# Performance work log

Hardware: AMD Instinct MI355X
Metric: run time of the kernel (lower is better)

The kernel has to match this reference:

```python
import jax, jax.numpy as jnp
import numpy as np

VOCAB = 32000
UNITS = 1024


def setup_inputs() -> dict:
    key = jax.random.key(0)
    ks = jax.random.split(key, 8)
    B, S, U = 64, 256, UNITS
    x = jax.random.randint(ks[0], (B, S), 0, VOCAB)
    emb = jax.random.normal(ks[1], (VOCAB, U), dtype=jnp.float32) * 0.02
    def gru_params(k):
        k1, k2, k3 = jax.random.split(k, 3)
        kernel = jax.random.normal(k1, (U, 3 * U), dtype=jnp.float32) * (1.0 / np.sqrt(U))
        rec_kernel = jax.random.normal(k2, (U, 3 * U), dtype=jnp.float32) * (1.0 / np.sqrt(U))
        bias = jnp.zeros((2, 3 * U), dtype=jnp.float32)  # reset_after=True: input bias + recurrent bias
        return kernel, rec_kernel, bias
    kf, rf, bf = gru_params(ks[2])
    kb, rb, bb = gru_params(ks[3])
    return {"x": x, "emb": emb,
            "kernel_fwd": kf, "rec_fwd": rf, "bias_fwd": bf,
            "kernel_bwd": kb, "rec_bwd": rb, "bias_bwd": bb}


def _gru(x_emb, mask, kernel, rec_kernel, bias, reverse):
    # Keras GRU, reset_after=True: z,r,hh gates; mask_zero copy-through state.
    if reverse:
        x_emb = x_emb[:, ::-1]
        mask = mask[:, ::-1]
    B, S, U = x_emb.shape
    b_i, b_r = bias[0], bias[1]
    # precompute input projections for all timesteps: [S, B, 3U]
    xp = (jnp.einsum('bsu,uh->bsh', x_emb, kernel) + b_i).transpose(1, 0, 2)
    mask_t = mask.transpose(1, 0)  # [S, B]

    def step(h, inp):
        xp_t, m_t = inp
        rec = h @ rec_kernel + b_r
        xz, xr, xh = jnp.split(xp_t, 3, axis=-1)
        rz, rr, rh = jnp.split(rec, 3, axis=-1)
        z = jax.nn.sigmoid(xz + rz)
        r = jax.nn.sigmoid(xr + rr)
        hh = jnp.tanh(xh + r * rh)
        h_new = z * h + (1.0 - z) * hh
        h = jnp.where(m_t[:, None], h_new, h)  # masked steps carry state/output through
        return h, h

    h0 = jnp.zeros((B, U), dtype=x_emb.dtype)
    _, outs = jax.lax.scan(step, h0, (xp, mask_t))
    outs = outs.transpose(1, 0, 2)  # [B, S, U]
    if reverse:
        outs = outs[:, ::-1]
    return outs


def reference(x, emb, kernel_fwd, rec_fwd, bias_fwd, kernel_bwd, rec_bwd, bias_bwd):
    mask = x != 0  # Embedding(mask_zero=True)
    x_emb = emb[x]  # [B, S, U]
    out_f = _gru(x_emb, mask, kernel_fwd, rec_fwd, bias_fwd, reverse=False)
    out_b = _gru(x_emb, mask, kernel_bwd, rec_bwd, bias_bwd, reverse=True)
    return out_f + out_b  # merge_mode='sum'
```

## Files before the change

### kernel.cpp

```cpp
#include <hip/hip_runtime.h>

typedef __bf16 bf16;
typedef __bf16 bf16x8 __attribute__((ext_vector_type(8)));
typedef __bf16 bf16x4 __attribute__((ext_vector_type(4)));
typedef float f32x4 __attribute__((ext_vector_type(4)));

static constexpr size_t SZ_RT   = 2ull*3072*1024*2;
static constexpr size_t SZ_XP   = 2ull*16384*3072*2;
static constexpr size_t SZ_MASK = 16384ull*4;
static constexpr size_t SLOT    = 2ull*8192*16;
static constexpr size_t OFF_RT   = 0;
static constexpr size_t OFF_XP   = OFF_RT + SZ_RT;
static constexpr size_t OFF_MASK = OFF_XP + SZ_XP;
static constexpr size_t OFF_BAR  = OFF_MASK + SZ_MASK;
static constexpr size_t OFF_RING = OFF_BAR + 2048;
static constexpr size_t OFF_KT   = OFF_RING;
static constexpr size_t OFF_XE   = OFF_RING + 2ull*3072*1024*2;

__global__ void zero_ws_k(char* ws) {
  size_t i = (size_t)blockIdx.x*256 + threadIdx.x;
  if (i < SLOT/16)                  ((uint4*)(ws + OFF_RING))[i] = make_uint4(0u,0u,0u,0u);
  else if (i < SLOT/16 + 128)       ((uint4*)(ws + OFF_BAR))[i - SLOT/16] = make_uint4(0u,0u,0u,0u);
}

__global__ void transpose_cast_k(const float* kf, const float* kb,
                                 const float* rf, const float* rb, char* ws) {
  __shared__ float tile[32][33];
  const int mat = blockIdx.z;
  const float* src = (mat==0)?kf:(mat==1)?kb:(mat==2)?rf:rb;
  bf16* dst = (bf16*)(ws + ((mat<2)?OFF_KT:OFF_RT)) + (size_t)(mat&1)*3072*1024;
  const int k0 = blockIdx.x*32, n0 = blockIdx.y*32;
  const int r = threadIdx.x >> 5, c = threadIdx.x & 31;
  for (int rr = r; rr < 32; rr += 8)
    tile[rr][c] = src[(size_t)(k0+rr)*3072 + n0 + c];
  __syncthreads();
  const int rn = threadIdx.x >> 3, kq = threadIdx.x & 7;
  bf16x4 v;
  #pragma unroll
  for (int ii = 0; ii < 4; ++ii) v[ii] = (bf16)tile[kq*4+ii][rn];
  *(bf16x4*)(dst + (size_t)(n0+rn)*1024 + k0 + kq*4) = v;
}

__global__ void gather_xe_k(const int* x, const float* emb, char* ws) {
  size_t c = (size_t)blockIdx.x*256 + threadIdx.x;
  int rowid = (int)(c >> 7); int u8 = (int)(c & 127);
  int t = rowid >> 6, b = rowid & 63;
  int tok = x[b*256 + t];
  const float* e = emb + (size_t)tok*1024 + u8*8;
  float4 a  = *(const float4*)e;
  float4 b2 = *(const float4*)(e+4);
  bf16x8 o;
  o[0]=(bf16)a.x;  o[1]=(bf16)a.y;  o[2]=(bf16)a.z;  o[3]=(bf16)a.w;
  o[4]=(bf16)b2.x; o[5]=(bf16)b2.y; o[6]=(bf16)b2.z; o[7]=(bf16)b2.w;
  *(bf16x8*)((bf16*)(ws+OFF_XE) + (size_t)rowid*1024 + u8*8) = o;
}

__global__ void make_mask_k(const int* x, char* ws) {
  int tid = blockIdx.x*256 + threadIdx.x;
  int t = tid >> 6, b = tid & 63;
  ((float*)(ws+OFF_MASK))[tid] = (x[b*256+t] != 0) ? 1.0f : 0.0f;
}

__device__ __forceinline__ void async16(void* lds, const void* g) {
  __builtin_amdgcn_global_load_lds((const __attribute__((address_space(1))) unsigned int*)g,
                                   (__attribute__((address_space(3))) unsigned int*)lds,
                                   16, 0, 0);
}

__global__ __launch_bounds__(256) void xp_gemm_k(const float* bias_f, const float* bias_b, char* ws) {
  __shared__ __align__(16) char smem[16384];
  const int tid = threadIdx.x, w = tid>>6, l = tid&63;
  const int m0 = blockIdx.x*128, n0 = blockIdx.y*128, d = blockIdx.z;
  const bf16* xe = (const bf16*)(ws + OFF_XE);
  const bf16* Bt = (const bf16*)(ws + OFF_KT) + (size_t)d*3072*1024;
  const float* bias = d ? bias_b : bias_f;
  const int wm = (w>>1)*64, wn = (w&1)*64;
  const f32x4 fzero = {0.f,0.f,0.f,0.f};
  f32x4 acc[4][4];
  #pragma unroll
  for (int i=0;i<4;++i)
    #pragma unroll
    for (int jj=0;jj<4;++jj) acc[i][jj] = fzero;
  for (int k0 = 0; k0 < 1024; k0 += 32) {
    #pragma unroll
    for (int it = 0; it < 2; ++it) {
      int cc = w*128 + it*64 + l;
      int row = cc>>2, kp = cc&3;
      async16(smem        + (size_t)(w*128 + it*64)*16, xe + (size_t)(m0+row)*1024 + k0 + kp*8);
      async16(smem + 8192 + (size_t)(w*128 + it*64)*16, Bt + (size_t)(n0+row)*1024 + k0 + kp*8);
    }
    __builtin_amdgcn_s_waitcnt(0);
    __syncthreads();
    const bf16* As = (const bf16*)smem;
    const bf16* Bs = (const bf16*)(smem + 8192);
    bf16x8 bfr[4];
    #pragma unroll
    for (int nt=0;nt<4;++nt)
      bfr[nt] = *(const bf16x8*)(Bs + (wn + nt*16 + (l&15))*32 + (l>>4)*8);
    #pragma unroll
    for (int mt=0;mt<4;++mt) {
      bf16x8 af = *(const bf16x8*)(As + (wm + mt*16 + (l&15))*32 + (l>>4)*8);
      #pragma unroll
      for (int nt=0;nt<4;++nt)
        acc[mt][nt] = __builtin_amdgcn_mfma_f32_16x16x32_bf16(af, bfr[nt], acc[mt][nt], 0,0,0);
    }
    __syncthreads();
  }
  bf16* xp = (bf16*)(ws + OFF_XP);
  #pragma unroll
  for (int nt=0;nt<4;++nt) {
    int n = n0 + wn + nt*16 + (l&15);
    float bv = bias[n];
    int g = n>>10, jj = (n>>4)&63, u = n&15;
    #pragma unroll
    for (int mt=0;mt<4;++mt) {
      #pragma unroll
      for (int r2=0;r2<4;++r2) {
        int m = m0 + wm + mt*16 + (l>>4)*4 + r2;
        int t = m>>6, b = m&63;
        float val = acc[mt][nt][r2] + bv;
        xp[((((size_t)(d*64+jj)*256 + t)*3 + g)*64 + b)*16 + u] = (bf16)val;
      }
    }
  }
}

__global__ __launch_bounds__(256, 1) void gru_scan_k(char* ws,
                                                     const float* bias_f, const float* bias_b) {
  __shared__ __align__(16) float parts[2*4*3*64*20];
  const int wg = blockIdx.x;
  const int d = wg >> 6, j = wg & 63;
  const int tid = threadIdx.x, w = tid >> 6, l = tid & 63;
  const bf16* rT    = (const bf16*)(ws + OFF_RT) + (size_t)d*3072*1024;
  const char* xp    = (const char*)(ws + OFF_XP);
  const float* mask = (const float*)(ws + OFF_MASK);
  char* ring = ws + OFF_RING;
  unsigned* flags = (unsigned*)(ws + OFF_BAR);
  const float* bias = d ? bias_b : bias_f;
  const f32x4 fzero = {0.f,0.f,0.f,0.f};

  const int b = tid >> 2, uq = tid & 3;

  f32x4 br[3];
  #pragma unroll
  for (int g = 0; g < 3; ++g)
    br[g] = *(const f32x4*)(bias + 3072 + g*1024 + j*16 + uq*4);

  const int kt0 = w*8;
  bf16x8 Breg[24];
  #pragma unroll
  for (int g = 0; g < 3; ++g)
    #pragma unroll
    for (int kk = 0; kk < 8; ++kk)
      Breg[g*8+kk] = *(const bf16x8*)(rT + (size_t)(g*1024 + j*16 + (l&15))*1024
                                         + (kt0+kk)*32 + (l>>4)*8);

  float hold[4] = {0.f, 0.f, 0.f, 0.f};

  const int wq = (j&1)*2 + (uq>>1);
  const int chunk = ((j>>1)*4 + (b>>4))*64 + ((b & 15) | (wq << 4));
  const int coff = chunk*16 + (uq&1)*8;

  const unsigned fidx = (unsigned)(d*256 + w*64 + l);

  bf16x4 xz_c, xr_c, xh_c; float m_c;
  {
    const int t0 = d ? 255 : 0;
    const char* xpt = xp + ((size_t)(d*64 + j)*256 + t0)*6144;
    xz_c = *(const bf16x4*)(xpt +        tid*8);
    xr_c = *(const bf16x4*)(xpt + 2048 + tid*8);
    xh_c = *(const bf16x4*)(xpt + 4096 + tid*8);
    m_c  = mask[t0*64 + b];
  }

  for (int step = 0; step < 256; ++step) {
    const int t = d ? (255 - step) : step;
    {
      unsigned v = __hip_atomic_load(&flags[fidx], __ATOMIC_RELAXED, __HIP_MEMORY_SCOPE_AGENT);
      while (!__all((int)(v >= (unsigned)step))) {
        __builtin_amdgcn_s_sleep(2);
        v = __hip_atomic_load(&flags[fidx], __ATOMIC_RELAXED, __HIP_MEMORY_SCOPE_AGENT);
      }
    }
    const char* hsrc = ring + (size_t)step*SLOT + (size_t)d*(SLOT/2);
    f32x4 acc[4][3];
    #pragma unroll
    for (int mt=0;mt<4;++mt) { acc[mt][0]=fzero; acc[mt][1]=fzero; acc[mt][2]=fzero; }
    bf16x8 aP[4], aN[4];
    #pragma unroll
    for (int mt=0;mt<4;++mt)
      aP[mt] = *(const bf16x8*)(hsrc + ((size_t)(kt0*4 + mt)*64 + l)*16);
    #pragma unroll
    for (int kk = 0; kk < 8; ++kk) {
      if (kk < 7) {
        #pragma unroll
        for (int mt=0;mt<4;++mt)
          aN[mt] = *(const bf16x8*)(hsrc + ((size_t)((kt0+kk+1)*4 + mt)*64 + l)*16);
      }
      #pragma unroll
      for (int mt = 0; mt < 4; ++mt) {
        acc[mt][0] = __builtin_amdgcn_mfma_f32_16x16x32_bf16(aP[mt], Breg[0*8+kk], acc[mt][0],0,0,0);
        acc[mt][1] = __builtin_amdgcn_mfma_f32_16x16x32_bf16(aP[mt], Breg[1*8+kk], acc[mt][1],0,0,0);
        acc[mt][2] = __builtin_amdgcn_mfma_f32_16x16x32_bf16(aP[mt], Breg[2*8+kk], acc[mt][2],0,0,0);
      }
      if (kk < 7) {
        #pragma unroll
        for (int mt=0;mt<4;++mt) aP[mt] = aN[mt];
      }
    }
    {
      float* pw = parts + ((size_t)((step&1)*4 + w)*3)*1280;
      #pragma unroll
      for (int mt = 0; mt < 4; ++mt)
        #pragma unroll
        for (int g = 0; g < 3; ++g)
          #pragma unroll
          for (int r2 = 0; r2 < 4; ++r2)
            pw[g*1280 + (mt*16 + (l>>4)*4 + r2)*20 + (l&15)] = acc[mt][g][r2];
    }
    __syncthreads();
    f32x4 rec0 = br[0], rec1 = br[1], rec2 = br[2];
    {
      const float* pb = parts + (size_t)(step&1)*4*3*1280 + b*20 + uq*4;
      #pragma unroll
      for (int w2 = 0; w2 < 4; ++w2) {
        rec0 += *(const f32x4*)(pb + (w2*3+0)*1280);
        rec1 += *(const f32x4*)(pb + (w2*3+1)*1280);
        rec2 += *(const f32x4*)(pb + (w2*3+2)*1280);
      }
    }
    f32x4 hv;
    #pragma unroll
    for (int i = 0; i < 4; ++i) {
      float z = 1.f/(1.f + __expf(-((float)xz_c[i] + rec0[i])));
      float r = 1.f/(1.f + __expf(-((float)xr_c[i] + rec1[i])));
      float pre = (float)xh_c[i] + r*rec2[i];
      pre = fminf(fmaxf(pre, -15.f), 15.f);
      float e2 = __expf(-2.f*pre);
      float hh = (1.f - e2)/(1.f + e2);
      float hn = z*hold[i] + (1.f - z)*hh;
      float ho = (m_c != 0.f) ? hn : hold[i];
      hold[i] = ho;
      hv[i] = ho;
    }
    if (step < 255) {
      union { bf16 h4[4]; unsigned long long q; } pk;
      #pragma unroll
      for (int i = 0; i < 4; ++i) pk.h4[i] = (bf16)hv[i];
      char* hdst = ring + (size_t)(step+1)*SLOT + (size_t)d*(SLOT/2);
      __hip_atomic_store((unsigned long long*)(hdst + coff), pk.q,
                         __ATOMIC_RELAXED, __HIP_MEMORY_SCOPE_AGENT);
      __builtin_amdgcn_s_waitcnt(0);
      asm volatile("" ::: "memory");
      if ((tid & 63) == 0)
        __hip_atomic_store(&flags[d*256 + j*4 + w], (unsigned)(step+1),
                           __ATOMIC_RELAXED, __HIP_MEMORY_SCOPE_AGENT);
    }
    {
      float* slab = (float*)(ws + OFF_XP + ((size_t)(d*64 + j)*256 + t)*6144);
      *(f32x4*)(slab + tid*4) = hv;
    }
    if (step < 255) {
      const int tn = d ? (254 - step) : (step + 1);
      const char* xpn = xp + ((size_t)(d*64 + j)*256 + tn)*6144;
      xz_c = *(const bf16x4*)(xpn +        tid*8);
      xr_c = *(const bf16x4*)(xpn + 2048 + tid*8);
      xh_c = *(const bf16x4*)(xpn + 4096 + tid*8);
      m_c  = mask[tn*64 + b];
    }
  }
}

__global__ void add_out_k(const char* ws, float* out) {
  size_t i = (size_t)blockIdx.x*256 + threadIdx.x;
  int uqq = (int)(i & 3), j = (int)((i>>2) & 63), t = (int)((i>>8) & 255), b = (int)(i >> 16);
  const float* pf = (const float*)(ws + OFF_XP + ((size_t)(     j)*256 + t)*6144);
  const float* pb = (const float*)(ws + OFF_XP + ((size_t)(64 + j)*256 + t)*6144);
  f32x4 a = *(const f32x4*)(pf + b*16 + uqq*4);
  f32x4 c = *(const f32x4*)(pb + b*16 + uqq*4);
  *(f32x4*)(out + ((size_t)b*256 + t)*1024 + j*16 + uqq*4) = a + c;
}

extern "C" void kernel_launch(void* const* d_in, const int* in_sizes, int n_in,
                              void* d_out, int out_size, void* d_ws, size_t ws_size,
                              hipStream_t stream) {
  (void)in_sizes; (void)n_in; (void)out_size; (void)ws_size;
  const int*   x   = (const int*)d_in[0];
  const float* emb = (const float*)d_in[1];
  const float* kf  = (const float*)d_in[2];
  const float* rf  = (const float*)d_in[3];
  const float* bf_ = (const float*)d_in[4];
  const float* kb  = (const float*)d_in[5];
  const float* rb  = (const float*)d_in[6];
  const float* bb  = (const float*)d_in[7];
  char* ws = (char*)d_ws;
  float* out = (float*)d_out;
  transpose_cast_k<<<dim3(32,96,4), 256, 0, stream>>>(kf, kb, rf, rb, ws);
  gather_xe_k<<<8192, 256, 0, stream>>>(x, emb, ws);
  make_mask_k<<<64, 256, 0, stream>>>(x, ws);
  xp_gemm_k<<<dim3(128,24,2), 256, 0, stream>>>(bf_, bb, ws);
  zero_ws_k<<<65, 256, 0, stream>>>(ws);
  gru_scan_k<<<128, 256, 0, stream>>>(ws, bf_, bb);
  add_out_k<<<16384, 256, 0, stream>>>(ws, out);
}
```

Measured before the change: 2.132 ms.

## Replace per-step flag barrier with NaN-sentinel polling on ring data

The recurrent scan no longer publishes and polls per-wave step flags. Instead the whole hidden-state ring is pre-filled with a bf16 NaN sentinel, and each wave loads its A fragments directly. It re-polls only the 16-byte chunks that still hold the sentinel, using atomic loads. This removes the s_waitcnt(0) and flag-store round trip from the serial 256-step critical path, so consumers can start as soon as the data lands. In exchange, a much larger fill kernel writes the full 257-slot ring before the scan, and correctness depends on the hidden state never producing the sentinel bit pattern.

After: 4.012 ms. 1.88x slower.

```diff
diff --git a/kernel.cpp b/kernel.cpp
--- a/kernel.cpp
+++ b/kernel.cpp
@@ -4,6 +4,7 @@
 typedef __bf16 bf16x8 __attribute__((ext_vector_type(8)));
 typedef __bf16 bf16x4 __attribute__((ext_vector_type(4)));
 typedef float f32x4 __attribute__((ext_vector_type(4)));
+typedef unsigned long long u64;
 
 static constexpr size_t SZ_RT   = 2ull*3072*1024*2;
 static constexpr size_t SZ_XP   = 2ull*16384*3072*2;
@@ -17,10 +18,15 @@
 static constexpr size_t OFF_KT   = OFF_RING;
 static constexpr size_t OFF_XE   = OFF_RING + 2ull*3072*1024*2;
 
-__global__ void zero_ws_k(char* ws) {
+static constexpr unsigned SENT    = 0x7fc0u;
+static constexpr unsigned SENT2   = 0x7fc07fc0u;
+
+__global__ void fill_ring_k(char* ws) {
   size_t i = (size_t)blockIdx.x*256 + threadIdx.x;
-  if (i < SLOT/16)                  ((uint4*)(ws + OFF_RING))[i] = make_uint4(0u,0u,0u,0u);
-  else if (i < SLOT/16 + 128)       ((uint4*)(ws + OFF_BAR))[i - SLOT/16] = make_uint4(0u,0u,0u,0u);
+  const size_t n0 = SLOT/16;
+  const size_t n  = 257ull*SLOT/16;
+  if (i < n0)      ((uint4*)(ws + OFF_RING))[i] = make_uint4(0u,0u,0u,0u);
+  else if (i < n)  ((uint4*)(ws + OFF_RING))[i] = make_uint4(SENT2,SENT2,SENT2,SENT2);
 }
 
 __global__ void transpose_cast_k(const float* kf, const float* kb,
@@ -135,7 +141,6 @@
   const char* xp    = (const char*)(ws + OFF_XP);
   const float* mask = (const float*)(ws + OFF_MASK);
   char* ring = ws + OFF_RING;
-  unsigned* flags = (unsigned*)(ws + OFF_BAR);
   const float* bias = d ? bias_b : bias_f;
   const f32x4 fzero = {0.f,0.f,0.f,0.f};
 
@@ -160,8 +165,6 @@
   const int wq = (j&1)*2 + (uq>>1);
   const int chunk = ((j>>1)*4 + (b>>4))*64 + ((b & 15) | (wq << 4));
   const int coff = chunk*16 + (uq&1)*8;
-
-  const unsigned fidx = (unsigned)(d*256 + w*64 + l);
 
   bf16x4 xz_c, xr_c, xh_c; float m_c;
   {
@@ -175,39 +178,42 @@
 
   for (int step = 0; step < 256; ++step) {
     const int t = d ? (255 - step) : step;
-    {
-      unsigned v = __hip_atomic_load(&flags[fidx], __ATOMIC_RELAXED, __HIP_MEMORY_SCOPE_AGENT);
-      while (!__all((int)(v >= (unsigned)step))) {
-        __builtin_amdgcn_s_sleep(2);
-        v = __hip_atomic_load(&flags[fidx], __ATOMIC_RELAXED, __HIP_MEMORY_SCOPE_AGENT);
+    const char* hsrc = ring + (size_t)step*SLOT + (size_t)d*(SLOT/2);
+
+    uint4 A[32];
+    #pragma unroll
+    for (int kk = 0; kk < 8; ++kk)
+      #pragma unroll
+      for (int mt = 0; mt < 4; ++mt)
+        A[kk*4+mt] = *(const uint4*)(hsrc + ((size_t)((kt0+kk)*4 + mt)*64 + l)*16);
+
+    #pragma unroll
+    for (int c = 0; c < 32; ++c) {
+      const char* cp = hsrc + ((size_t)(kt0*4 + c)*64 + l)*16;
+      int st = (int)(((A[c].x & 0xffffu) == SENT) | ((A[c].z & 0xffffu) == SENT));
+      while (__any(st)) {
+        u64 lo = __hip_atomic_load((const u64*)cp,       __ATOMIC_RELAXED, __HIP_MEMORY_SCOPE_AGENT);
+        u64 hi = __hip_atomic_load((const u64*)(cp + 8), __ATOMIC_RELAXED, __HIP_MEMORY_SCOPE_AGENT);
+        A[c].x = (unsigned)lo; A[c].y = (unsigned)(lo >> 32);
+        A[c].z = (unsigned)hi; A[c].w = (unsigned)(hi >> 32);
+        st = (int)(((A[c].x & 0xffffu) == SENT) | ((A[c].z & 0xffffu) == SENT));
       }
     }
-    const char* hsrc = ring + (size_t)step*SLOT + (size_t)d*(SLOT/2);
+
     f32x4 acc[4][3];
     #pragma unroll
     for (int mt=0;mt<4;++mt) { acc[mt][0]=fzero; acc[mt][1]=fzero; acc[mt][2]=fzero; }
-    bf16x8 aP[4], aN[4];
-    #pragma unroll
-    for (int mt=0;mt<4;++mt)
-      aP[mt] = *(const bf16x8*)(hsrc + ((size_t)(kt0*4 + mt)*64 + l)*16);
     #pragma unroll
     for (int kk = 0; kk < 8; ++kk) {
-      if (kk < 7) {
-        #pragma unroll
-        for (int mt=0;mt<4;++mt)
-          aN[mt] = *(const bf16x8*)(hsrc + ((size_t)((kt0+kk+1)*4 + mt)*64 + l)*16);
+      #pragma unroll
+      for (int mt = 0; mt < 4; ++mt) {
+        bf16x8 a = __builtin_bit_cast(bf16x8, A[kk*4+mt]);
+        acc[mt][0] = __builtin_amdgcn_mfma_f32_16x16x32_bf16(a, Breg[0*8+kk], acc[mt][0],0,0,0);
+        acc[mt][1] = __builtin_amdgcn_mfma_f32_16x16x32_bf16(a, Breg[1*8+kk], acc[mt][1],0,0,0);
+        acc[mt][2] = __builtin_amdgcn_mfma_f32_16x16x32_bf16(a, Breg[2*8+kk], acc[mt][2],0,0,0);
       }
-      #pragma unroll
-      for (int mt = 0; mt < 4; ++mt) {
-        acc[mt][0] = __builtin_amdgcn_mfma_f32_16x16x32_bf16(aP[mt], Breg[0*8+kk], acc[mt][0],0,0,0);
-        acc[mt][1] = __builtin_amdgcn_mfma_f32_16x16x32_bf16(aP[mt], Breg[1*8+kk], acc[mt][1],0,0,0);
-        acc[mt][2] = __builtin_amdgcn_mfma_f32_16x16x32_bf16(aP[mt], Breg[2*8+kk], acc[mt][2],0,0,0);
-      }
-      if (kk < 7) {
-        #pragma unroll
-        for (int mt=0;mt<4;++mt) aP[mt] = aN[mt];
-      }
-    }
+    }
+
     {
       float* pw = parts + ((size_t)((step&1)*4 + w)*3)*1280;
       #pragma unroll
@@ -219,6 +225,7 @@
             pw[g*1280 + (mt*16 + (l>>4)*4 + r2)*20 + (l&15)] = acc[mt][g][r2];
     }
     __syncthreads();
+
     f32x4 rec0 = br[0], rec1 = br[1], rec2 = br[2];
     {
       const float* pb = parts + (size_t)(step&1)*4*3*1280 + b*20 + uq*4;
@@ -243,23 +250,21 @@
       hold[i] = ho;
       hv[i] = ho;
     }
+
     if (step < 255) {
-      union { bf16 h4[4]; unsigned long long q; } pk;
+      union { bf16 h4[4]; u64 q; } pk;
       #pragma unroll
       for (int i = 0; i < 4; ++i) pk.h4[i] = (bf16)hv[i];
       char* hdst = ring + (size_t)(step+1)*SLOT + (size_t)d*(SLOT/2);
-      __hip_atomic_store((unsigned long long*)(hdst + coff), pk.q,
+      __hip_atomic_store((u64*)(hdst + coff), pk.q,
                          __ATOMIC_RELAXED, __HIP_MEMORY_SCOPE_AGENT);
-      __builtin_amdgcn_s_waitcnt(0);
-      asm volatile("" ::: "memory");
-      if ((tid & 63) == 0)
-        __hip_atomic_store(&flags[d*256 + j*4 + w], (unsigned)(step+1),
-                           __ATOMIC_RELAXED, __HIP_MEMORY_SCOPE_AGENT);
-    }
+    }
+
     {
       float* slab = (float*)(ws + OFF_XP + ((size_t)(d*64 + j)*256 + t)*6144);
       *(f32x4*)(slab + tid*4) = hv;
     }
+
     if (step < 255) {
       const int tn = d ? (254 - step) : (step + 1);
       const char* xpn = xp + ((size_t)(d*64 + j)*256 + tn)*6144;
@@ -299,7 +304,7 @@
   gather_xe_k<<<8192, 256, 0, stream>>>(x, emb, ws);
   make_mask_k<<<64, 256, 0, stream>>>(x, ws);
   xp_gemm_k<<<dim3(128,24,2), 256, 0, stream>>>(bf_, bb, ws);
-  zero_ws_k<<<65, 256, 0, stream>>>(ws);
+  fill_ring_k<<<16448, 256, 0, stream>>>(ws);
   gru_scan_k<<<128, 256, 0, stream>>>(ws, bf_, bb);
   add_out_k<<<16384, 256, 0, stream>>>(ws, out);
 }
```
